# Optimization experiments

Hardware: AMD Instinct MI355X
Metric: run time of the kernel (lower is better)

## Reference

```python
import jax, jax.numpy as jnp
import numpy as np
from jax import lax

B, T_CAP, V, E, D = 64, 32, 32000, 1024, 1024  # embed_dim == encoder_dim required by the module


def _lstm_cell(x, h, c, W_ih, W_hh, b_ih, b_hh):
    # gates: [B, 4D]; PyTorch LSTMCell gate order: i, f, g, o
    gates = x @ W_ih.T + b_ih + h @ W_hh.T + b_hh
    i, f, g, o = jnp.split(gates, 4, axis=-1)
    c_new = jax.nn.sigmoid(f) * c + jax.nn.sigmoid(i) * jnp.tanh(g)
    h_new = jax.nn.sigmoid(o) * jnp.tanh(c_new)
    return h_new, c_new


def setup_inputs() -> dict:
    key = jax.random.key(0)
    ks = jax.random.split(key, 9)
    encoder_out = jax.random.normal(ks[0], (B, E), jnp.float32)
    encoded_captions = jax.random.randint(ks[1], (B, T_CAP), 0, V, dtype=jnp.int64)
    caption_lengths = jax.random.randint(ks[2], (B, 1), 2, T_CAP + 1, dtype=jnp.int64)
    caption_lengths = caption_lengths.at[0, 0].set(T_CAP)  # ensure max decode len = T_CAP-1 (static)
    s = 1.0 / np.sqrt(D).astype(np.float32)
    embedding = jax.random.normal(ks[3], (V, E), jnp.float32)
    W_ih = jax.random.uniform(ks[4], (4 * D, E), jnp.float32, -s, s)
    W_hh = jax.random.uniform(ks[5], (4 * D, D), jnp.float32, -s, s)
    b_ih = jax.random.uniform(ks[6], (4 * D,), jnp.float32, -s, s)
    b_hh = jax.random.uniform(ks[7], (4 * D,), jnp.float32, -s, s)
    fc_W = jax.random.uniform(ks[8], (V, D), jnp.float32, -0.1, 0.1)  # reset_parameters
    fc_b = jnp.zeros((V,), jnp.float32)
    return {"encoder_out": encoder_out, "encoded_captions": encoded_captions,
            "caption_lengths": caption_lengths, "embedding": embedding,
            "W_ih": W_ih, "W_hh": W_hh, "b_ih": b_ih, "b_hh": b_hh,
            "fc_W": fc_W, "fc_b": fc_b}


def reference(encoder_out, encoded_captions, caption_lengths, embedding,
              W_ih, W_hh, b_ih, b_hh, fc_W, fc_b):
    lengths = caption_lengths[:, 0]
    sort_ind = jnp.argsort(-lengths)  # descending, stable (matches torch sort semantics)
    lengths = lengths[sort_ind]
    enc = encoder_out[sort_ind]                       # [B, E]
    caps = encoded_captions[sort_ind]                 # [B, T]
    emb = embedding[caps]                             # [B, T, E]
    decode_lengths = lengths - 1                      # [B]
    t_dec = emb.shape[1] - 1                          # static = T_CAP - 1

    zeros = jnp.zeros((enc.shape[0], D), enc.dtype)
    h, c = _lstm_cell(enc, zeros, zeros, W_ih, W_hh, b_ih, b_hh)  # warm-up step with encoder_out

    # masked update is equivalent to the torch :batch_size_t slicing because
    # lengths are sorted descending -> the active prefix only shrinks over t.
    masks = jnp.arange(t_dec)[:, None] < decode_lengths[None, :]  # [T-1, B]
    xs = jnp.swapaxes(emb[:, :t_dec], 0, 1)                       # [T-1, B, E]

    def step(carry, inp):
        h, c = carry
        x_t, m = inp
        hn, cn = _lstm_cell(x_t, h, c, W_ih, W_hh, b_ih, b_hh)
        m2 = m[:, None]
        h = jnp.where(m2, hn, h)
        c = jnp.where(m2, cn, c)
        # dropout in eval mode == identity
        preds = (h @ fc_W.T + fc_b) * m2.astype(h.dtype)  # inactive rows stay 0
        return (h, c), preds

    (_, _), preds = lax.scan(step, (h, c), (xs, masks))
    predictions = jnp.swapaxes(preds, 0, 1)  # [B, T-1, V]
    return predictions, decode_lengths, sort_ind
```

## Files before the change

### kernel.cpp

```cpp
#include <hip/hip_runtime.h>
#include <cstddef>
#include <cstdint>

#define PRED_N 63488000

typedef unsigned short u16;
typedef unsigned long long u64;
typedef __attribute__((ext_vector_type(8))) unsigned short us8;
typedef __attribute__((ext_vector_type(4))) float f32x4;
typedef __attribute__((ext_vector_type(8))) __bf16 bf16x8;

__device__ __forceinline__ float bf2f(u16 h){
  unsigned u = ((unsigned)h) << 16;
  return __builtin_bit_cast(float, u);
}
__device__ __forceinline__ u16 f2bf(float f){
  unsigned u = __builtin_bit_cast(unsigned, f);
  u += 0x7FFFu + ((u >> 16) & 1u);
  return (u16)(u >> 16);
}
__device__ __forceinline__ float sigf(float x){ return 1.f/(1.f + __expf(-x)); }
__device__ __forceinline__ float tanhf_(float x){ return 1.f - 2.f/(__expf(2.f*x) + 1.f); }

__device__ __forceinline__ f32x4 mfma16(us8 a, us8 b, f32x4 c){
  return __builtin_amdgcn_mfma_f32_16x16x32_bf16(
      __builtin_bit_cast(bf16x8, a), __builtin_bit_cast(bf16x8, b), c, 0, 0, 0);
}
__device__ __forceinline__ u64 pack4bf(const float* h){
  return (u64)f2bf(h[0]) | ((u64)f2bf(h[1]) << 16)
       | ((u64)f2bf(h[2]) << 32) | ((u64)f2bf(h[3]) << 48);
}
__device__ __forceinline__ us8 pack8(float4 a, float4 b){
  us8 r;
  r[0]=f2bf(a.x); r[1]=f2bf(a.y); r[2]=f2bf(a.z); r[3]=f2bf(a.w);
  r[4]=f2bf(b.x); r[5]=f2bf(b.y); r[6]=f2bf(b.z); r[7]=f2bf(b.w);
  return r;
}
__device__ __forceinline__ float ldf(const void* p, int f32, int i){
  return f32 ? ((const float*)p)[i] : bf2f(((const u16*)p)[i]);
}
__device__ __forceinline__ int ldi(const int* p, int i64, int i){
  return i64 ? p[2*i] : p[i];
}

__global__ void k_detect(const unsigned* __restrict__ embw, const int* __restrict__ lenw,
                         int* __restrict__ flags){
  if(threadIdx.x == 0){
    int hits = 0;
    for(int i = 0; i < 16; ++i){
      unsigned w = embw[i];
      int elo = (w >> 7) & 0xFF, ehi = (w >> 23) & 0xFF;
      hits += (elo >= 112 && elo <= 133) && (ehi >= 112 && ehi <= 133);
    }
    flags[0] = (hits >= 12) ? 0 : 1;
    int orv = 0;
    for(int i = 0; i < 4; ++i) orv |= lenw[2*i + 1];
    flags[1] = (orv == 0) ? 1 : 0;
  }
}

__global__ void k_setup(const int* __restrict__ lens, int* __restrict__ wsI,
                        const int* __restrict__ flags, void* __restrict__ out){
  const int i = threadIdx.x;
  const int f32 = flags[0], i64 = flags[1];
  const int li = ldi(lens, i64, i);
  int rank = 0;
  for(int j = 0; j < 64; ++j){
    const int lj = ldi(lens, i64, j);
    rank += (lj > li) || (lj == li && j < i);
  }
  wsI[rank]      = i;
  wsI[64 + rank] = li - 1;
  if(f32){
    ((float*)out)[PRED_N + rank]      = (float)(li - 1);
    ((float*)out)[PRED_N + 64 + rank] = (float)i;
  } else {
    ((u16*)out)[PRED_N + rank]      = f2bf((float)(li - 1));
    ((u16*)out)[PRED_N + 64 + rank] = f2bf((float)i);
  }
}

__global__ void __launch_bounds__(256) k_conv16(const void* __restrict__ W,
    const int* __restrict__ flags, u16* __restrict__ dst, int n8){
  const int f32 = flags[0];
  const int stride = gridDim.x * 256;
  for(int i = blockIdx.x * 256 + threadIdx.x; i < n8; i += stride){
    if(f32){
      const float4* s = (const float4*)W + 2 * (size_t)i;
      ((us8*)dst)[i] = pack8(s[0], s[1]);
    } else {
      ((uint4*)dst)[i] = ((const uint4*)W)[i];
    }
  }
}

__global__ void __launch_bounds__(256) k_gather(const void* __restrict__ enc,
    const int* __restrict__ caps, const void* __restrict__ emb,
    const int* __restrict__ wsI, const int* __restrict__ flags, u16* __restrict__ X){
  const int r = blockIdx.x, t = r >> 6, b = r & 63;
  const int f32 = flags[0], i64 = flags[1];
  const int sb = wsI[b];
  const size_t rowoff = (t == 0) ? (size_t)sb * 1024
                                 : (size_t)ldi(caps, i64, sb * 32 + (t - 1)) * 1024;
  const void* base = (t == 0) ? enc : emb;
  u16* dst = X + (size_t)r * 1024;
  if(f32){
    const float4* src = (const float4*)((const float*)base + rowoff);
    float4 v = src[threadIdx.x];
    u64 w = (u64)f2bf(v.x) | ((u64)f2bf(v.y) << 16)
          | ((u64)f2bf(v.z) << 32) | ((u64)f2bf(v.w) << 48);
    ((u64*)dst)[threadIdx.x] = w;
  } else {
    const uint2* src = (const uint2*)((const u16*)base + rowoff);
    ((uint2*)dst)[threadIdx.x] = src[threadIdx.x];
  }
}

__device__ __forceinline__ void gemm_main(const u16* __restrict__ A, const void* __restrict__ Bv,
    int bF32, int arowmax, u16* As, u16* Bs, f32x4 (&acc)[4][4]){
  const int tid = threadIdx.x, wave = tid >> 6, lane = tid & 63;
  const int mq = (wave >> 1) * 64, nq = (wave & 1) * 64;
  const int l15 = lane & 15, lq = lane >> 4;
  const int r0 = lane >> 2, c0 = (lane & 3) * 8;
  const u16* Bb = (const u16*)Bv; const float* Bf = (const float*)Bv;
  for(int k0 = 0; k0 < 1024; k0 += 32){
    us8 av[2], bv[2];
#pragma unroll
    for(int c2 = 0; c2 < 2; ++c2){
      const int chunk = wave * 2 + c2;
      int ar = chunk * 16 + r0; if(ar > arowmax) ar = arowmax;
      av[c2] = *(const us8*)(A + (size_t)ar * 1024 + k0 + c0);
      const size_t bo = (size_t)(chunk * 16 + r0) * 1024 + k0 + c0;
      if(bF32){
        const float* p = Bf + bo;
        bv[c2] = pack8(*(const float4*)p, *(const float4*)(p + 4));
      } else {
        bv[c2] = *(const us8*)(Bb + bo);
      }
    }
    __syncthreads();
#pragma unroll
    for(int c2 = 0; c2 < 2; ++c2){
      const int chunk = wave * 2 + c2;
      *(us8*)&As[chunk * 512 + r0 * 32 + c0] = av[c2];
      *(us8*)&Bs[chunk * 512 + r0 * 32 + c0] = bv[c2];
    }
    __syncthreads();
    us8 af[4], bfv[4];
#pragma unroll
    for(int i = 0; i < 4; ++i){
      af[i]  = *(const us8*)&As[(mq + i * 16 + l15) * 32 + lq * 8];
      bfv[i] = *(const us8*)&Bs[(nq + i * 16 + l15) * 32 + lq * 8];
    }
#pragma unroll
    for(int i = 0; i < 4; ++i)
#pragma unroll
      for(int j = 0; j < 4; ++j)
        acc[i][j] = mfma16(af[i], bfv[j], acc[i][j]);
  }
}

__global__ void __launch_bounds__(256) k_gemm_gates(const u16* __restrict__ X,
    const u16* __restrict__ Wih16, const void* __restrict__ bih, const void* __restrict__ bhh,
    const int* __restrict__ flags, float* __restrict__ gatesx){
  __shared__ u16 As[4096], Bs[4096];
  const int tid = threadIdx.x, wave = tid >> 6, lane = tid & 63;
  const int bm = blockIdx.x, bn = blockIdx.y;
  const int mq = (wave >> 1) * 64, nq = (wave & 1) * 64;
  const int l15 = lane & 15, lq = lane >> 4;
  const int f32 = flags[0];
  f32x4 acc[4][4] = {};
  gemm_main(X + (size_t)bm * 128 * 1024, Wih16 + (size_t)bn * 128 * 1024, 0, 127, As, Bs, acc);
  const int rowb = bm * 128 + mq, colb = bn * 128 + nq;
#pragma unroll
  for(int j = 0; j < 4; ++j){
    const int col = colb + j * 16 + l15;
    const float bias = ldf(bih, f32, col) + ldf(bhh, f32, col);
#pragma unroll
    for(int i = 0; i < 4; ++i)
#pragma unroll
      for(int v = 0; v < 4; ++v){
        const int row = rowb + i * 16 + lq * 4 + v;
        gatesx[(size_t)row * 4096 + col] = acc[i][j][v] + bias;
      }
  }
}

__global__ void __launch_bounds__(256) k_init(const float* __restrict__ gatesx,
    u16* __restrict__ Hbuf, float* __restrict__ Cbuf){
  const int m = blockIdx.x, d0 = threadIdx.x * 4;
  const float* gx = gatesx + (size_t)m * 4096 + d0;
  f32x4 iv = *(const f32x4*)(gx);
  f32x4 gv = *(const f32x4*)(gx + 2048);
  f32x4 ov = *(const f32x4*)(gx + 3072);
  f32x4 cv; float h[4];
#pragma unroll
  for(int e = 0; e < 4; ++e){
    const float cn = sigf(iv[e]) * tanhf_(gv[e]);
    cv[e] = cn;
    h[e] = sigf(ov[e]) * tanhf_(cn);
  }
  *(f32x4*)(Cbuf + (size_t)m * 1024 + d0) = cv;
  *(u64*)(Hbuf + (size_t)m * 1024 + d0) = pack4bf(h);
}

__global__ void __launch_bounds__(256) k_step2(const u16* __restrict__ Whh16,
    const float* __restrict__ gatesx, const int* __restrict__ wsI,
    u16* __restrict__ Hbuf, float* __restrict__ Cbuf, int t){
  __shared__ float red[4096];
  const int tid = threadIdx.x, wave = tid >> 6, lane = tid & 63, blk = blockIdx.x;
  const int l15 = lane & 15, lq = lane >> 4;
  const int brow = (l15 >> 2) * 1024 + blk * 4 + (l15 & 3);
  const u16* Bp = Whh16 + (size_t)brow * 1024 + wave * 256 + lq * 8;
  const u16* Ap = Hbuf + (size_t)t * 65536 + wave * 256 + lq * 8;
  f32x4 acc[4] = {};
#pragma unroll
  for(int kt = 0; kt < 8; ++kt){
    const us8 bw = *(const us8*)(Bp + kt * 32);
#pragma unroll
    for(int mi = 0; mi < 4; ++mi){
      const us8 af = *(const us8*)(Ap + (size_t)(mi * 16 + l15) * 1024 + kt * 32);
      acc[mi] = mfma16(af, bw, acc[mi]);
    }
  }
#pragma unroll
  for(int mi = 0; mi < 4; ++mi)
#pragma unroll
    for(int v = 0; v < 4; ++v)
      red[wave * 1024 + (mi * 16 + lq * 4 + v) * 16 + l15] = acc[mi][v];
  __syncthreads();

  const int m = tid >> 2, dr = tid & 3;
  const int dim = blk * 4 + dr;
  const int dlm = wsI[64 + m];
  const float* gx = gatesx + ((size_t)(t + 1) * 64 + m) * 4096 + dim;
  float g4[4];
#pragma unroll
  for(int g = 0; g < 4; ++g){
    const int n = g * 4 + dr;
    g4[g] = red[m * 16 + n] + red[1024 + m * 16 + n]
          + red[2048 + m * 16 + n] + red[3072 + m * 16 + n]
          + gx[(size_t)g * 1024];
  }
  u16* hdst = Hbuf + ((size_t)(t + 1) * 64 + m) * 1024 + dim;
  if(t < dlm){
    float* cp = Cbuf + (size_t)m * 1024 + dim;
    const float cn = sigf(g4[1]) * (*cp) + sigf(g4[0]) * tanhf_(g4[2]);
    *cp = cn;
    *hdst = f2bf(sigf(g4[3]) * tanhf_(cn));
  } else {
    *hdst = Hbuf[((size_t)t * 64 + m) * 1024 + dim];
  }
}

__global__ void __launch_bounds__(256) k_gemm_fc(const u16* __restrict__ H,
    const void* __restrict__ fcW, const u16* __restrict__ fcW16, const int useW16,
    const void* __restrict__ fcb, const int* __restrict__ declen,
    const int* __restrict__ flags, void* __restrict__ out){
  __shared__ u16 As[4096], Bs[4096];
  const int tid = threadIdx.x, wave = tid >> 6, lane = tid & 63;
  const int bid = blockIdx.x;
  const int L = (bid & 7) * 500 + (bid >> 3);
  const int bm = L & 15, bn = L >> 4;
  const int mq = (wave >> 1) * 64, nq = (wave & 1) * 64;
  const int l15 = lane & 15, lq = lane >> 4;
  const int f32 = flags[0];
  const int bf32 = useW16 ? 0 : f32;
  f32x4 acc[4][4] = {};
  const int amax0 = 1983 - bm * 128;
  const void* Bbase = useW16 ? (const void*)(fcW16 + (size_t)bn * 128 * 1024)
      : (f32 ? (const void*)((const float*)fcW + (size_t)bn * 128 * 1024)
             : (const void*)((const u16*)fcW + (size_t)bn * 128 * 1024));
  gemm_main(H + (size_t)bm * 128 * 1024, Bbase, bf32,
            amax0 > 127 ? 127 : amax0, As, Bs, acc);
  const int rowb = bm * 128 + mq, colb = bn * 128 + nq;
  int   col[4];
  float bias[4];
#pragma unroll
  for(int j = 0; j < 4; ++j){
    col[j] = colb + j * 16 + l15;
    bias[j] = ldf(fcb, f32, col[j]);
  }
#pragma unroll
  for(int i = 0; i < 4; ++i)
#pragma unroll
    for(int v = 0; v < 4; ++v){
      const int row = rowb + i * 16 + lq * 4 + v;
      if(row < 1984){
        const int t = row >> 6, b = row & 63;
        const bool act = (t < declen[b]);
        const size_t obase = (size_t)b * 992000 + (size_t)t * 32000;
#pragma unroll
        for(int j = 0; j < 4; ++j){
          const float val = act ? (acc[i][j][v] + bias[j]) : 0.f;
          if(f32) ((float*)out)[obase + col[j]] = val;
          else    ((u16*)out)[obase + col[j]] = f2bf(val);
        }
      }
    }
}

extern "C" void kernel_launch(void* const* d_in, const int* in_sizes, int n_in,
                              void* d_out, int out_size, void* d_ws, size_t ws_size,
                              hipStream_t stream){
  const void* enc = d_in[0];
  const int*  caps = (const int*)d_in[1];
  const int*  lens = (const int*)d_in[2];
  const void* emb = d_in[3];
  const void* Wih = d_in[4];
  const void* Whh = d_in[5];
  const void* bih = d_in[6];
  const void* bhh = d_in[7];
  const void* fcW = d_in[8];
  const void* fcb = d_in[9];

  float* gatesx = (float*)d_out;
  u16*   Xbuf   = (u16*)((char*)d_out + (size_t)32*1024*1024);
  u16*   Whh16  = (u16*)((char*)d_out + (size_t)36*1024*1024);
  u16*   Wih16  = (u16*)((char*)d_out + (size_t)36*1024*1024 + 8388608);
  char* ws = (char*)d_ws;
  int*   flags = (int*)ws;
  int*   wsI   = (int*)(ws + 256);
  float* Cbuf  = (float*)(ws + 1024);
  u16*   Hbuf  = (u16*)(ws + (size_t)512*1024);
  u16*   fcW16 = (u16*)(ws + (size_t)8*1024*1024);
  const int useFc16 = (ws_size >= (size_t)74*1024*1024) ? 1 : 0;

  hipLaunchKernelGGL(k_detect, dim3(1), dim3(64), 0, stream,
                     (const unsigned*)emb, lens, flags);
  hipLaunchKernelGGL(k_setup, dim3(1), dim3(64), 0, stream, lens, wsI, flags, d_out);
  hipLaunchKernelGGL(k_conv16, dim3(2048), dim3(256), 0, stream, Wih, flags, Wih16, 524288);
  hipLaunchKernelGGL(k_conv16, dim3(2048), dim3(256), 0, stream, Whh, flags, Whh16, 524288);
  if(useFc16)
    hipLaunchKernelGGL(k_conv16, dim3(4096), dim3(256), 0, stream, fcW, flags, fcW16, 4096000);
  hipLaunchKernelGGL(k_gather, dim3(2048), dim3(256), 0, stream, enc, caps, emb, wsI, flags, Xbuf);
  hipLaunchKernelGGL(k_gemm_gates, dim3(16, 32), dim3(256), 0, stream, Xbuf, Wih16, bih, bhh, flags, gatesx);
  hipLaunchKernelGGL(k_init, dim3(64), dim3(256), 0, stream, gatesx, Hbuf, Cbuf);
  for(int t = 0; t < 31; ++t)
    hipLaunchKernelGGL(k_step2, dim3(256), dim3(256), 0, stream, Whh16, gatesx, wsI, Hbuf, Cbuf, t);
  hipLaunchKernelGGL(k_gemm_fc, dim3(4000), dim3(256), 0, stream,
                     Hbuf + (size_t)64 * 1024, fcW, fcW16, useFc16, fcb, wsI + 64, flags, d_out);
}
```

Before: 925.1 us.

## Fuse LSTM recurrence into one persistent cooperative kernel with register-resident W_hh

The init kernel and the 31 per-step launches are replaced by a single cooperative kernel of 64 blocks. Each block keeps its slice of W_hh in registers and its cell state in registers, and uses a grid-wide sync between timesteps. This removes per-step launch overhead and the repeated reloading of W_hh. The GEMM shared-memory tiles also get an XOR swizzle to reduce LDS bank conflicts. In exchange, only 64 of the GPU's CUs run the recurrence, grid.sync latency is paid every step, and the 32 us8 register arrays raise register pressure.

```diff
diff --git a/kernel.cpp b/kernel.cpp
--- a/kernel.cpp
+++ b/kernel.cpp
@@ -1,6 +1,9 @@
 #include <hip/hip_runtime.h>
+#include <hip/hip_cooperative_groups.h>
 #include <cstddef>
 #include <cstdint>
+
+namespace cg = cooperative_groups;
 
 #define PRED_N 63488000
 
@@ -122,6 +125,8 @@
   const int mq = (wave >> 1) * 64, nq = (wave & 1) * 64;
   const int l15 = lane & 15, lq = lane >> 4;
   const int r0 = lane >> 2, c0 = (lane & 3) * 8;
+  const int sww = ((r0 & 7) << 3);
+  const int swr = ((l15 & 7) << 3);
   const u16* Bb = (const u16*)Bv; const float* Bf = (const float*)Bv;
   for(int k0 = 0; k0 < 1024; k0 += 32){
     us8 av[2], bv[2];
@@ -142,15 +147,15 @@
 #pragma unroll
     for(int c2 = 0; c2 < 2; ++c2){
       const int chunk = wave * 2 + c2;
-      *(us8*)&As[chunk * 512 + r0 * 32 + c0] = av[c2];
-      *(us8*)&Bs[chunk * 512 + r0 * 32 + c0] = bv[c2];
+      *(us8*)&As[(chunk * 512 + r0 * 32 + c0) ^ sww] = av[c2];
+      *(us8*)&Bs[(chunk * 512 + r0 * 32 + c0) ^ sww] = bv[c2];
     }
     __syncthreads();
     us8 af[4], bfv[4];
 #pragma unroll
     for(int i = 0; i < 4; ++i){
-      af[i]  = *(const us8*)&As[(mq + i * 16 + l15) * 32 + lq * 8];
-      bfv[i] = *(const us8*)&Bs[(nq + i * 16 + l15) * 32 + lq * 8];
+      af[i]  = *(const us8*)&As[((mq + i * 16 + l15) * 32 + lq * 8) ^ swr];
+      bfv[i] = *(const us8*)&Bs[((nq + i * 16 + l15) * 32 + lq * 8) ^ swr];
     }
 #pragma unroll
     for(int i = 0; i < 4; ++i)
@@ -186,70 +191,75 @@
   }
 }
 
-__global__ void __launch_bounds__(256) k_init(const float* __restrict__ gatesx,
-    u16* __restrict__ Hbuf, float* __restrict__ Cbuf){
-  const int m = blockIdx.x, d0 = threadIdx.x * 4;
-  const float* gx = gatesx + (size_t)m * 4096 + d0;
-  f32x4 iv = *(const f32x4*)(gx);
-  f32x4 gv = *(const f32x4*)(gx + 2048);
-  f32x4 ov = *(const f32x4*)(gx + 3072);
-  f32x4 cv; float h[4];
-#pragma unroll
-  for(int e = 0; e < 4; ++e){
-    const float cn = sigf(iv[e]) * tanhf_(gv[e]);
-    cv[e] = cn;
-    h[e] = sigf(ov[e]) * tanhf_(cn);
-  }
-  *(f32x4*)(Cbuf + (size_t)m * 1024 + d0) = cv;
-  *(u64*)(Hbuf + (size_t)m * 1024 + d0) = pack4bf(h);
-}
-
-__global__ void __launch_bounds__(256) k_step2(const u16* __restrict__ Whh16,
+__global__ void __launch_bounds__(256, 1) k_rnn(const u16* __restrict__ Whh16,
     const float* __restrict__ gatesx, const int* __restrict__ wsI,
-    u16* __restrict__ Hbuf, float* __restrict__ Cbuf, int t){
-  __shared__ float red[4096];
+    u16* __restrict__ Hbuf){
+  __shared__ __align__(16) float gl[4096];
+  cg::grid_group grid = cg::this_grid();
   const int tid = threadIdx.x, wave = tid >> 6, lane = tid & 63, blk = blockIdx.x;
   const int l15 = lane & 15, lq = lane >> 4;
-  const int brow = (l15 >> 2) * 1024 + blk * 4 + (l15 & 3);
-  const u16* Bp = Whh16 + (size_t)brow * 1024 + wave * 256 + lq * 8;
-  const u16* Ap = Hbuf + (size_t)t * 65536 + wave * 256 + lq * 8;
-  f32x4 acc[4] = {};
-#pragma unroll
-  for(int kt = 0; kt < 8; ++kt){
-    const us8 bw = *(const us8*)(Bp + kt * 32);
-#pragma unroll
-    for(int mi = 0; mi < 4; ++mi){
-      const us8 af = *(const us8*)(Ap + (size_t)(mi * 16 + l15) * 1024 + kt * 32);
-      acc[mi] = mfma16(af, bw, acc[mi]);
-    }
-  }
-#pragma unroll
-  for(int mi = 0; mi < 4; ++mi)
-#pragma unroll
-    for(int v = 0; v < 4; ++v)
-      red[wave * 1024 + (mi * 16 + lq * 4 + v) * 16 + l15] = acc[mi][v];
-  __syncthreads();
-
-  const int m = tid >> 2, dr = tid & 3;
-  const int dim = blk * 4 + dr;
-  const int dlm = wsI[64 + m];
-  const float* gx = gatesx + ((size_t)(t + 1) * 64 + m) * 4096 + dim;
-  float g4[4];
-#pragma unroll
-  for(int g = 0; g < 4; ++g){
-    const int n = g * 4 + dr;
-    g4[g] = red[m * 16 + n] + red[1024 + m * 16 + n]
-          + red[2048 + m * 16 + n] + red[3072 + m * 16 + n]
-          + gx[(size_t)g * 1024];
-  }
-  u16* hdst = Hbuf + ((size_t)(t + 1) * 64 + m) * 1024 + dim;
-  if(t < dlm){
-    float* cp = Cbuf + (size_t)m * 1024 + dim;
-    const float cn = sigf(g4[1]) * (*cp) + sigf(g4[0]) * tanhf_(g4[2]);
-    *cp = cn;
-    *hdst = f2bf(sigf(g4[3]) * tanhf_(cn));
-  } else {
-    *hdst = Hbuf[((size_t)t * 64 + m) * 1024 + dim];
+  const int m = tid >> 2, d4 = (tid & 3) * 4;
+  const int dl = wsI[64 + m];
+
+  float c4[4], h4[4];
+  {
+    const float* gx0 = gatesx + (size_t)m * 4096 + blk * 16 + d4;
+    f32x4 iv = *(const f32x4*)(gx0);
+    f32x4 gv = *(const f32x4*)(gx0 + 2048);
+    f32x4 ov = *(const f32x4*)(gx0 + 3072);
+#pragma unroll
+    for(int e = 0; e < 4; ++e){
+      c4[e] = sigf(iv[e]) * tanhf_(gv[e]);
+      h4[e] = sigf(ov[e]) * tanhf_(c4[e]);
+    }
+    *(u64*)(Hbuf + (size_t)m * 1024 + blk * 16 + d4) = pack4bf(h4);
+  }
+  us8 breg[32];
+  {
+    const u16* Bp = Whh16 + ((size_t)wave * 1024 + blk * 16 + l15) * 1024 + lq * 8;
+#pragma unroll
+    for(int kt = 0; kt < 32; ++kt) breg[kt] = *(const us8*)(Bp + kt * 32);
+  }
+  __threadfence();
+  grid.sync();
+
+#pragma unroll 1
+  for(int t = 0; t < 31; ++t){
+    f32x4 acc[4] = {};
+    const u16* Ht = Hbuf + (size_t)t * 65536 + lq * 8;
+#pragma unroll
+    for(int kt = 0; kt < 32; ++kt){
+#pragma unroll
+      for(int mi = 0; mi < 4; ++mi){
+        const us8 af = *(const us8*)(Ht + (size_t)(mi * 16 + l15) * 1024 + kt * 32);
+        acc[mi] = mfma16(af, breg[kt], acc[mi]);
+      }
+    }
+#pragma unroll
+    for(int mi = 0; mi < 4; ++mi)
+#pragma unroll
+      for(int v = 0; v < 4; ++v)
+        gl[wave * 1024 + (mi * 16 + lq * 4 + v) * 16 + l15] = acc[mi][v];
+    __syncthreads();
+
+    const float* gx = gatesx + ((size_t)(t + 1) * 64 + m) * 4096 + blk * 16 + d4;
+    f32x4 gg[4];
+#pragma unroll
+    for(int g = 0; g < 4; ++g){
+      f32x4 s = *(const f32x4*)&gl[g * 1024 + m * 16 + d4];
+      gg[g] = s + *(const f32x4*)(gx + (size_t)g * 1024);
+    }
+    if(t < dl){
+#pragma unroll
+      for(int e = 0; e < 4; ++e){
+        const float cn = sigf(gg[1][e]) * c4[e] + sigf(gg[0][e]) * tanhf_(gg[2][e]);
+        c4[e] = cn;
+        h4[e] = sigf(gg[3][e]) * tanhf_(cn);
+      }
+    }
+    *(u64*)(Hbuf + ((size_t)(t + 1) * 64 + m) * 1024 + blk * 16 + d4) = pack4bf(h4);
+    __threadfence();
+    grid.sync();
   }
 }
 
@@ -321,7 +331,6 @@
   char* ws = (char*)d_ws;
   int*   flags = (int*)ws;
   int*   wsI   = (int*)(ws + 256);
-  float* Cbuf  = (float*)(ws + 1024);
   u16*   Hbuf  = (u16*)(ws + (size_t)512*1024);
   u16*   fcW16 = (u16*)(ws + (size_t)8*1024*1024);
   const int useFc16 = (ws_size >= (size_t)74*1024*1024) ? 1 : 0;
@@ -335,9 +344,13 @@
     hipLaunchKernelGGL(k_conv16, dim3(4096), dim3(256), 0, stream, fcW, flags, fcW16, 4096000);
   hipLaunchKernelGGL(k_gather, dim3(2048), dim3(256), 0, stream, enc, caps, emb, wsI, flags, Xbuf);
   hipLaunchKernelGGL(k_gemm_gates, dim3(16, 32), dim3(256), 0, stream, Xbuf, Wih16, bih, bhh, flags, gatesx);
-  hipLaunchKernelGGL(k_init, dim3(64), dim3(256), 0, stream, gatesx, Hbuf, Cbuf);
-  for(int t = 0; t < 31; ++t)
-    hipLaunchKernelGGL(k_step2, dim3(256), dim3(256), 0, stream, Whh16, gatesx, wsI, Hbuf, Cbuf, t);
+
+  {
+    const u16* a0 = Whh16; const float* a1 = gatesx; const int* a2 = wsI; u16* a3 = Hbuf;
+    void* kargs[] = {(void*)&a0, (void*)&a1, (void*)&a2, (void*)&a3};
+    hipLaunchCooperativeKernel((const void*)k_rnn, dim3(64), dim3(256), kargs, 0, stream);
+  }
+
   hipLaunchKernelGGL(k_gemm_fc, dim3(4000), dim3(256), 0, stream,
                      Hbuf + (size_t)64 * 1024, fcW, fcW16, useFc16, fcb, wsI + 64, flags, d_out);
 }
```

After: 1.825 ms. +97.3%, slower.
